# Kernel tuning notes

Hardware: AMD Instinct MI355X
Metric: run time of the kernel (lower is better)

## Reference

```python
import jax, jax.numpy as jnp
import numpy as np

N = 100000
E = 6400000
NT_DIM = 8
HID = 32


def setup_inputs() -> dict:
    key = jax.random.key(0)
    k1, k2, k3, k4, k5, k6, k7 = jax.random.split(key, 7)
    nt_emb = jax.random.normal(k1, (N, NT_DIM), dtype=jnp.float32)
    edge_index = jax.random.randint(k2, (2, E), 0, N, dtype=jnp.int64)
    lm_mask = jax.random.uniform(k3, (N,), dtype=jnp.float32)
    fan_in1 = 2 * NT_DIM + 2
    lim1 = 1.0 / np.sqrt(fan_in1)
    W1 = jax.random.uniform(k4, (fan_in1, HID), minval=-lim1, maxval=lim1, dtype=jnp.float32)
    b1 = jax.random.uniform(k5, (HID,), minval=-lim1, maxval=lim1, dtype=jnp.float32)
    lim2 = 1.0 / np.sqrt(HID)
    W2 = jax.random.uniform(k6, (HID, 1), minval=-lim2, maxval=lim2, dtype=jnp.float32)
    b2 = jax.random.uniform(k7, (1,), minval=-lim2, maxval=lim2, dtype=jnp.float32)
    return {"nt_emb": nt_emb, "edge_index": edge_index, "lm_mask": lm_mask,
            "W1": W1, "b1": b1, "W2": W2, "b2": b2}


def reference(nt_emb, edge_index, lm_mask, W1, b1, W2, b2):
    s, d = edge_index[0], edge_index[1]
    # [E, 2*nt_dim + 2] edge features: src emb, dst emb, src mask, dst mask
    feat = jnp.concatenate(
        [nt_emb[s], nt_emb[d], lm_mask[s][:, None], lm_mask[d][:, None]], axis=-1)
    h = jax.nn.relu(feat @ W1 + b1)          # [E, hid]
    out = jax.nn.sigmoid(h @ W2 + b2)        # [E, 1]
    return out[:, 0]                         # [E]
```

## Files before the change

### kernel.cpp

```cpp
#include <hip/hip_runtime.h>
#include <hip/hip_bf16.h>

typedef short short8 __attribute__((ext_vector_type(8)));
typedef float floatx4 __attribute__((ext_vector_type(4)));
typedef float floatx16 __attribute__((ext_vector_type(16)));

#define HID 32
#define NTD 8
#define FAN_IN 18

__device__ __forceinline__ short f2bf(float f) {
    union { float f; unsigned u; } v; v.f = f;
    unsigned r = v.u + 0x7fffu + ((v.u >> 16) & 1u);
    return (short)(r >> 16);
}

__device__ __forceinline__ float fast_sigmoid(float x) {
    float e = __builtin_amdgcn_exp2f(x * -1.44269504f);
    return __builtin_amdgcn_rcpf(1.0f + e);
}

__global__ void build_table(const float* __restrict__ emb,
                            const float* __restrict__ mask,
                            short* __restrict__ T, int N) {
    int n = blockIdx.x * blockDim.x + threadIdx.x;
    if (n >= N) return;
    const float4* p = (const float4*)(emb + (size_t)n * NTD);
    float4 lo = p[0], hi = p[1];
    short8 a, b;
    a[0] = f2bf(lo.x); a[1] = f2bf(lo.y); a[2] = f2bf(lo.z); a[3] = f2bf(lo.w);
    a[4] = f2bf(hi.x); a[5] = f2bf(hi.y); a[6] = f2bf(hi.z); a[7] = f2bf(hi.w);
    b[0] = f2bf(mask[n]); b[1] = (short)0x3F80;
    b[2] = b[3] = b[4] = b[5] = b[6] = b[7] = 0;
    short8* row = (short8*)(T + (size_t)n * 16);
    row[0] = a; row[1] = b;
}


__device__ __forceinline__ void make_frags(int4 lo, int4 hi, int h,
                                           short8& sf, short8& df) {
    int4 s4, d4;
    #pragma unroll
    for (int j = 0; j < 4; ++j) {
        int a = (&lo.x)[j];
        int b = (&hi.x)[j];
        int as = __shfl_xor(a, 32, 64);
        int bs = __shfl_xor(b, 32, 64);
        (&s4.x)[j] = h ? bs : a;
        (&d4.x)[j] = h ? b : as;
    }
    sf = __builtin_bit_cast(short8, s4);
    df = __builtin_bit_cast(short8, d4);
}

template <int ESZ>
__device__ __forceinline__ unsigned ld_idx(const char* __restrict__ idxBase,
                                           unsigned grp, unsigned nGroups,
                                           unsigned E, unsigned off, unsigned cc) {
    unsigned g = grp < nGroups ? grp : nGroups - 1u;
    unsigned e = g * 64u + off + cc;
    if (e >= E) e = E - 1u;
    return *(const unsigned*)(idxBase + (size_t)e * ESZ);
}

template <int ESZ>
__device__ void run32(const char* __restrict__ ei,
                      const char* __restrict__ Tc,
                      float* __restrict__ out, unsigned E,
                      short8 as, short8 ad, const float* __restrict__ w2r, float bias2,
                      unsigned waveId, unsigned nWaves, int h, int c, int lane) {
    const unsigned nGroups = (E + 63u) >> 6;
    const char* idxBase = ei + (h ? (size_t)E * ESZ : 0);
    const unsigned cc = (unsigned)c;

    if (waveId >= nGroups) return;
    unsigned cur = waveId;

    unsigned iA = ld_idx<ESZ>(idxBase, cur, nGroups, E, 0u, cc);
    unsigned iB = ld_idx<ESZ>(idxBase, cur, nGroups, E, 32u, cc);
    int4 loA = *(const int4*)(Tc + iA * 32u);
    int4 hiA = *(const int4*)(Tc + iA * 32u + 16u);
    int4 loB = *(const int4*)(Tc + iB * 32u);
    int4 hiB = *(const int4*)(Tc + iB * 32u + 16u);
    unsigned nA = ld_idx<ESZ>(idxBase, cur + nWaves, nGroups, E, 0u, cc);
    unsigned nB = ld_idx<ESZ>(idxBase, cur + nWaves, nGroups, E, 32u, cc);

    while (true) {
        int4 nloA = *(const int4*)(Tc + nA * 32u);
        int4 nhiA = *(const int4*)(Tc + nA * 32u + 16u);
        int4 nloB = *(const int4*)(Tc + nB * 32u);
        int4 nhiB = *(const int4*)(Tc + nB * 32u + 16u);
        unsigned nnA = ld_idx<ESZ>(idxBase, cur + 2u * nWaves, nGroups, E, 0u, cc);
        unsigned nnB = ld_idx<ESZ>(idxBase, cur + 2u * nWaves, nGroups, E, 32u, cc);

        short8 sfA, dfA, sfB, dfB;
        make_frags(loA, hiA, h, sfA, dfA);
        make_frags(loB, hiB, h, sfB, dfB);

        floatx16 accA = {0.f,0.f,0.f,0.f,0.f,0.f,0.f,0.f,0.f,0.f,0.f,0.f,0.f,0.f,0.f,0.f};
        floatx16 accB = accA;
        accA = __builtin_amdgcn_mfma_f32_32x32x16_bf16(as, sfA, accA, 0, 0, 0);
        accB = __builtin_amdgcn_mfma_f32_32x32x16_bf16(as, sfB, accB, 0, 0, 0);
        accA = __builtin_amdgcn_mfma_f32_32x32x16_bf16(ad, dfA, accA, 0, 0, 0);
        accB = __builtin_amdgcn_mfma_f32_32x32x16_bf16(ad, dfB, accB, 0, 0, 0);

        float pA0 = 0.f, pA1 = 0.f, pB0 = 0.f, pB1 = 0.f;
        #pragma unroll
        for (int q = 0; q < 16; q += 2) {
            pA0 += fmaxf(accA[q],     0.f) * w2r[q];
            pA1 += fmaxf(accA[q + 1], 0.f) * w2r[q + 1];
            pB0 += fmaxf(accB[q],     0.f) * w2r[q];
            pB1 += fmaxf(accB[q + 1], 0.f) * w2r[q + 1];
        }
        float pA = pA0 + pA1;
        float pB = pB0 + pB1;
        pA += __shfl_xor(pA, 32, 64);
        pB += __shfl_xor(pB, 32, 64);
        float vA = fast_sigmoid(pA + bias2);
        float vB = fast_sigmoid(pB + bias2);

        float v = (h == 0) ? vA : vB;
        unsigned e = (cur << 6) + (unsigned)lane;
        if (e < E) out[e] = v;

        cur += nWaves;
        if (cur >= nGroups) break;
        loA = nloA; hiA = nhiA; loB = nloB; hiB = nhiB;
        nA = nnA; nB = nnB;
    }
}

__global__ __launch_bounds__(256, 4) void lg_table_kernel(
    const char* __restrict__ ei_bytes,
    const short* __restrict__ T,
    const float* __restrict__ W1,
    const float* __restrict__ b1,
    const float* __restrict__ W2,
    const float* __restrict__ b2,
    float* __restrict__ out,
    long long E)
{
    const int lane = threadIdx.x & 63;
    const int waveInBlock = threadIdx.x >> 6;
    const unsigned waveId = (unsigned)(blockIdx.x * (blockDim.x >> 6) + waveInBlock);
    const unsigned nWaves = (unsigned)(gridDim.x * (blockDim.x >> 6));

    const int* ei32 = (const int*)ei_bytes;
    int probe = ei32[2 * lane + 1];
    unsigned long long nz = __ballot(probe != 0);
    const int esz = (nz == 0ull) ? 8 : 4;

    const int c = lane & 31;
    const int h = lane >> 5;

    short8 as, ad;
    #pragma unroll
    for (int j = 0; j < 8; ++j) {
        float vs = 0.f, vd = 0.f;
        if (h == 0) {
            vs = W1[j * HID + c];
            vd = W1[(8 + j) * HID + c];
        } else {
            if (j == 0) { vs = W1[16 * HID + c]; vd = W1[17 * HID + c]; }
            else if (j == 1) { vs = b1[c]; }
        }
        as[j] = f2bf(vs);
        ad[j] = f2bf(vd);
    }

    float w2r[16];
    #pragma unroll
    for (int q = 0; q < 16; ++q)
        w2r[q] = W2[(q & 3) + 8 * (q >> 2) + 4 * h];

    const float bias2 = b2[0];

    if (esz == 8)
        run32<8>(ei_bytes, (const char*)T, out, (unsigned)E, as, ad, w2r, bias2,
                 waveId, nWaves, h, c, lane);
    else
        run32<4>(ei_bytes, (const char*)T, out, (unsigned)E, as, ad, w2r, bias2,
                 waveId, nWaves, h, c, lane);
}

__global__ __launch_bounds__(256, 4) void lg_kernel(
    const float* __restrict__ nt_emb,
    const char* __restrict__ ei_bytes,
    const float* __restrict__ lm_mask,
    const float* __restrict__ W1,
    const float* __restrict__ b1,
    const float* __restrict__ W2,
    const float* __restrict__ b2,
    float* __restrict__ out,
    long long E)
{
    const int lane = threadIdx.x & 63;
    const int waveInBlock = threadIdx.x >> 6;
    const long long waveId = (long long)blockIdx.x * (blockDim.x >> 6) + waveInBlock;
    const long long nWaves = (long long)gridDim.x * (blockDim.x >> 6);

    const int* ei32 = (const int*)ei_bytes;
    int probe = ei32[2 * lane + 1];
    unsigned long long nz = __ballot(probe != 0);
    const long long esz = (nz == 0ull) ? 8 : 4;

    const int r = lane & 15;
    const int g = lane >> 4;

    short8 a0, a1;
    #pragma unroll
    for (int j = 0; j < 8; ++j) {
        int k = g * 8 + j;
        float v0 = 0.f, v1 = 0.f;
        if (k < FAN_IN)       { v0 = W1[k * HID + r];      v1 = W1[k * HID + 16 + r]; }
        else if (k == FAN_IN) { v0 = b1[r];                v1 = b1[16 + r]; }
        a0[j] = f2bf(v0);
        a1[j] = f2bf(v1);
    }

    float w2v0[4], w2v1[4];
    #pragma unroll
    for (int q = 0; q < 4; ++q) {
        w2v0[q] = W2[g * 4 + q];
        w2v1[q] = W2[16 + g * 4 + q];
    }
    const float bias2 = b2[0];

    const long long nGroups = (E + 15) >> 4;
    for (long long grp = waveId; grp < nGroups; grp += nWaves) {
        long long e = (grp << 4) + r;
        const bool valid = (e < E);
        long long ec = valid ? e : (E - 1);

        int s = *(const int*)(ei_bytes + ec * esz);
        int d = *(const int*)(ei_bytes + (E + ec) * esz);

        short8 fb;
        #pragma unroll
        for (int j = 0; j < 8; ++j) fb[j] = 0;
        if (g < 2) {
            const float4* p = (const float4*)(nt_emb + (long long)(g == 0 ? s : d) * NTD);
            float4 lo = p[0];
            float4 hi = p[1];
            fb[0] = f2bf(lo.x); fb[1] = f2bf(lo.y); fb[2] = f2bf(lo.z); fb[3] = f2bf(lo.w);
            fb[4] = f2bf(hi.x); fb[5] = f2bf(hi.y); fb[6] = f2bf(hi.z); fb[7] = f2bf(hi.w);
        } else if (g == 2) {
            fb[0] = f2bf(lm_mask[s]);
            fb[1] = f2bf(lm_mask[d]);
            fb[2] = (short)0x3F80;
        }

        floatx4 acc0 = {0.f, 0.f, 0.f, 0.f};
        floatx4 acc1 = {0.f, 0.f, 0.f, 0.f};
        acc0 = __builtin_amdgcn_mfma_f32_16x16x32_bf16(a0, fb, acc0, 0, 0, 0);
        acc1 = __builtin_amdgcn_mfma_f32_16x16x32_bf16(a1, fb, acc1, 0, 0, 0);

        float partial = 0.f;
        #pragma unroll
        for (int q = 0; q < 4; ++q) {
            partial += fmaxf(acc0[q], 0.f) * w2v0[q];
            partial += fmaxf(acc1[q], 0.f) * w2v1[q];
        }
        partial += __shfl_xor(partial, 16, 64);
        partial += __shfl_xor(partial, 32, 64);

        float val = fast_sigmoid(partial + bias2);
        if (g == 0 && valid) out[e] = val;
    }
}

extern "C" void kernel_launch(void* const* d_in, const int* in_sizes, int n_in,
                              void* d_out, int out_size, void* d_ws, size_t ws_size,
                              hipStream_t stream) {
    const float* nt_emb = (const float*)d_in[0];
    const char*  ei     = (const char*)d_in[1];
    const float* lm     = (const float*)d_in[2];
    const float* W1     = (const float*)d_in[3];
    const float* b1     = (const float*)d_in[4];
    const float* W2     = (const float*)d_in[5];
    const float* b2     = (const float*)d_in[6];
    float* out = (float*)d_out;

    long long E = (long long)in_sizes[1] / 2;
    int N = in_sizes[2];

    size_t tableBytes = (size_t)N * 32;
    if (ws_size >= tableBytes) {
        short* T = (short*)d_ws;
        build_table<<<dim3((N + 255) / 256), dim3(256), 0, stream>>>(nt_emb, lm, T, N);
        lg_table_kernel<<<dim3(2048), dim3(256), 0, stream>>>(ei, T, W1, b1, W2, b2, out, E);
    } else {
        lg_kernel<<<dim3(2048), dim3(256), 0, stream>>>(nt_emb, ei, lm, W1, b1, W2, b2, out, E);
    }
}
```

Before: 83.28 us.

## Pack node table into 16-byte rows with mask bits stolen from bf16 LSBs

The per-node gather table shrinks from 32 to 16 bytes by rounding embeddings to 15-bit bf16 and storing an 8-bit quantized mask in their low bits. Each edge lane now gathers one 16-byte row instead of two, and the MFMA fragments are rebuilt with only a mask shuffle. The W1 fragment layout is rearranged to match. This halves random-gather traffic at the cost of reduced embedding precision and an 8-bit mask quantization, plus some extra ALU for decoding.

```diff
diff --git a/kernel.cpp b/kernel.cpp
--- a/kernel.cpp
+++ b/kernel.cpp
@@ -15,6 +15,13 @@
     return (short)(r >> 16);
 }
 
+__device__ __forceinline__ unsigned short pack_emb(float f, unsigned bit) {
+    union { float f; unsigned u; } v; v.f = f;
+    unsigned r = v.u + 0xFFFFu + ((v.u >> 17) & 1u);
+    unsigned short s = (unsigned short)((r >> 16) & 0xFFFEu);
+    return (unsigned short)(s | bit);
+}
+
 __device__ __forceinline__ float fast_sigmoid(float x) {
     float e = __builtin_amdgcn_exp2f(x * -1.44269504f);
     return __builtin_amdgcn_rcpf(1.0f + e);
@@ -22,45 +29,76 @@
 
 __global__ void build_table(const float* __restrict__ emb,
                             const float* __restrict__ mask,
-                            short* __restrict__ T, int N) {
+                            unsigned short* __restrict__ T, int N) {
     int n = blockIdx.x * blockDim.x + threadIdx.x;
     if (n >= N) return;
     const float4* p = (const float4*)(emb + (size_t)n * NTD);
     float4 lo = p[0], hi = p[1];
-    short8 a, b;
-    a[0] = f2bf(lo.x); a[1] = f2bf(lo.y); a[2] = f2bf(lo.z); a[3] = f2bf(lo.w);
-    a[4] = f2bf(hi.x); a[5] = f2bf(hi.y); a[6] = f2bf(hi.z); a[7] = f2bf(hi.w);
-    b[0] = f2bf(mask[n]); b[1] = (short)0x3F80;
-    b[2] = b[3] = b[4] = b[5] = b[6] = b[7] = 0;
-    short8* row = (short8*)(T + (size_t)n * 16);
-    row[0] = a; row[1] = b;
-}
-
-
-__device__ __forceinline__ void make_frags(int4 lo, int4 hi, int h,
-                                           short8& sf, short8& df) {
-    int4 s4, d4;
-    #pragma unroll
-    for (int j = 0; j < 4; ++j) {
-        int a = (&lo.x)[j];
-        int b = (&hi.x)[j];
-        int as = __shfl_xor(a, 32, 64);
-        int bs = __shfl_xor(b, 32, 64);
-        (&s4.x)[j] = h ? bs : a;
-        (&d4.x)[j] = h ? b : as;
-    }
-    sf = __builtin_bit_cast(short8, s4);
-    df = __builtin_bit_cast(short8, d4);
-}
+    float ev[8] = {lo.x, lo.y, lo.z, lo.w, hi.x, hi.y, hi.z, hi.w};
+    float mf = mask[n] * 255.0f + 0.5f;
+    unsigned m8 = (unsigned)mf; if (m8 > 255u) m8 = 255u;
+    unsigned short row[8];
+    #pragma unroll
+    for (int j = 0; j < 8; ++j)
+        row[j] = pack_emb(ev[j], (m8 >> j) & 1u);
+    int4 out;
+    out.x = (int)((unsigned)row[0] | ((unsigned)row[1] << 16));
+    out.y = (int)((unsigned)row[2] | ((unsigned)row[3] << 16));
+    out.z = (int)((unsigned)row[4] | ((unsigned)row[5] << 16));
+    out.w = (int)((unsigned)row[6] | ((unsigned)row[7] << 16));
+    *(int4*)(T + (size_t)n * 8) = out;
+}
+
+__device__ __forceinline__ unsigned decode_m8(int4 r) {
+    unsigned m;
+    m  = ((unsigned)r.x & 1u);
+    m |= (((unsigned)r.x >> 16) & 1u) << 1;
+    m |= ((unsigned)r.y & 1u) << 2;
+    m |= (((unsigned)r.y >> 16) & 1u) << 3;
+    m |= ((unsigned)r.z & 1u) << 4;
+    m |= (((unsigned)r.z >> 16) & 1u) << 5;
+    m |= ((unsigned)r.w & 1u) << 6;
+    m |= (((unsigned)r.w >> 16) & 1u) << 7;
+    return m;
+}
+
 
 template <int ESZ>
-__device__ __forceinline__ unsigned ld_idx(const char* __restrict__ idxBase,
-                                           unsigned grp, unsigned nGroups,
-                                           unsigned E, unsigned off, unsigned cc) {
+__device__ __forceinline__ uint2 ld_idx2(const char* __restrict__ idxBase,
+                                         unsigned grp, unsigned nGroups,
+                                         unsigned E, unsigned cc) {
     unsigned g = grp < nGroups ? grp : nGroups - 1u;
-    unsigned e = g * 64u + off + cc;
-    if (e >= E) e = E - 1u;
-    return *(const unsigned*)(idxBase + (size_t)e * ESZ);
+    unsigned eA = g * 64u + cc;
+    unsigned eB = eA + 32u;
+    if (eA >= E) eA = E - 1u;
+    if (eB >= E) eB = E - 1u;
+    uint2 r;
+    r.x = *(const unsigned*)(idxBase + (size_t)eA * ESZ);
+    r.y = *(const unsigned*)(idxBase + (size_t)eB * ESZ);
+    return r;
+}
+
+__device__ __forceinline__ int4 grow(const char* __restrict__ Tc, unsigned idx) {
+    return *(const int4*)(Tc + (size_t)idx * 16u);
+}
+
+__device__ __forceinline__ void tile_frags(int4 row, int h, short8& fb1, short8& fb2) {
+    unsigned m8 = decode_m8(row);
+    unsigned m8p = (unsigned)__shfl_xor((int)m8, 32, 64);
+    float mfv = (float)m8p * (1.0f / 255.0f);
+    unsigned mbf = (unsigned)(unsigned short)f2bf(mfv);
+    int4 b1i, b2i;
+    if (h) {
+        b1i.x = (int)(mbf | 0x3F800000u);
+        b1i.y = 0; b1i.z = 0; b1i.w = 0;
+        b2i = row;
+    } else {
+        b1i = row;
+        b2i.x = (int)mbf;
+        b2i.y = 0; b2i.z = 0; b2i.w = 0;
+    }
+    fb1 = __builtin_bit_cast(short8, b1i);
+    fb2 = __builtin_bit_cast(short8, b2i);
 }
 
 template <int ESZ>
@@ -76,33 +114,26 @@
     if (waveId >= nGroups) return;
     unsigned cur = waveId;
 
-    unsigned iA = ld_idx<ESZ>(idxBase, cur, nGroups, E, 0u, cc);
-    unsigned iB = ld_idx<ESZ>(idxBase, cur, nGroups, E, 32u, cc);
-    int4 loA = *(const int4*)(Tc + iA * 32u);
-    int4 hiA = *(const int4*)(Tc + iA * 32u + 16u);
-    int4 loB = *(const int4*)(Tc + iB * 32u);
-    int4 hiB = *(const int4*)(Tc + iB * 32u + 16u);
-    unsigned nA = ld_idx<ESZ>(idxBase, cur + nWaves, nGroups, E, 0u, cc);
-    unsigned nB = ld_idx<ESZ>(idxBase, cur + nWaves, nGroups, E, 32u, cc);
+    uint2 i0 = ld_idx2<ESZ>(idxBase, cur, nGroups, E, cc);
+    int4 rA = grow(Tc, i0.x);
+    int4 rB = grow(Tc, i0.y);
+    uint2 i1 = ld_idx2<ESZ>(idxBase, cur + nWaves, nGroups, E, cc);
 
     while (true) {
-        int4 nloA = *(const int4*)(Tc + nA * 32u);
-        int4 nhiA = *(const int4*)(Tc + nA * 32u + 16u);
-        int4 nloB = *(const int4*)(Tc + nB * 32u);
-        int4 nhiB = *(const int4*)(Tc + nB * 32u + 16u);
-        unsigned nnA = ld_idx<ESZ>(idxBase, cur + 2u * nWaves, nGroups, E, 0u, cc);
-        unsigned nnB = ld_idx<ESZ>(idxBase, cur + 2u * nWaves, nGroups, E, 32u, cc);
-
-        short8 sfA, dfA, sfB, dfB;
-        make_frags(loA, hiA, h, sfA, dfA);
-        make_frags(loB, hiB, h, sfB, dfB);
+        int4 nA = grow(Tc, i1.x);
+        int4 nB = grow(Tc, i1.y);
+        uint2 i2 = ld_idx2<ESZ>(idxBase, cur + 2u * nWaves, nGroups, E, cc);
+
+        short8 fb1A, fb2A, fb1B, fb2B;
+        tile_frags(rA, h, fb1A, fb2A);
+        tile_frags(rB, h, fb1B, fb2B);
 
         floatx16 accA = {0.f,0.f,0.f,0.f,0.f,0.f,0.f,0.f,0.f,0.f,0.f,0.f,0.f,0.f,0.f,0.f};
         floatx16 accB = accA;
-        accA = __builtin_amdgcn_mfma_f32_32x32x16_bf16(as, sfA, accA, 0, 0, 0);
-        accB = __builtin_amdgcn_mfma_f32_32x32x16_bf16(as, sfB, accB, 0, 0, 0);
-        accA = __builtin_amdgcn_mfma_f32_32x32x16_bf16(ad, dfA, accA, 0, 0, 0);
-        accB = __builtin_amdgcn_mfma_f32_32x32x16_bf16(ad, dfB, accB, 0, 0, 0);
+        accA = __builtin_amdgcn_mfma_f32_32x32x16_bf16(as, fb1A, accA, 0, 0, 0);
+        accB = __builtin_amdgcn_mfma_f32_32x32x16_bf16(as, fb1B, accB, 0, 0, 0);
+        accA = __builtin_amdgcn_mfma_f32_32x32x16_bf16(ad, fb2A, accA, 0, 0, 0);
+        accB = __builtin_amdgcn_mfma_f32_32x32x16_bf16(ad, fb2B, accB, 0, 0, 0);
 
         float pA0 = 0.f, pA1 = 0.f, pB0 = 0.f, pB1 = 0.f;
         #pragma unroll
@@ -125,14 +156,14 @@
 
         cur += nWaves;
         if (cur >= nGroups) break;
-        loA = nloA; hiA = nhiA; loB = nloB; hiB = nhiB;
-        nA = nnA; nB = nnB;
+        rA = nA; rB = nB;
+        i1 = i2;
     }
 }
 
 __global__ __launch_bounds__(256, 4) void lg_table_kernel(
     const char* __restrict__ ei_bytes,
-    const short* __restrict__ T,
+    const unsigned short* __restrict__ T,
     const float* __restrict__ W1,
     const float* __restrict__ b1,
     const float* __restrict__ W2,
@@ -159,10 +190,11 @@
         float vs = 0.f, vd = 0.f;
         if (h == 0) {
             vs = W1[j * HID + c];
+            if (j == 0) vd = W1[17 * HID + c];
+        } else {
+            if (j == 0) vs = W1[16 * HID + c];
+            else if (j == 1) vs = b1[c];
             vd = W1[(8 + j) * HID + c];
-        } else {
-            if (j == 0) { vs = W1[16 * HID + c]; vd = W1[17 * HID + c]; }
-            else if (j == 1) { vs = b1[c]; }
         }
         as[j] = f2bf(vs);
         ad[j] = f2bf(vd);
@@ -284,9 +316,9 @@
     long long E = (long long)in_sizes[1] / 2;
     int N = in_sizes[2];
 
-    size_t tableBytes = (size_t)N * 32;
+    size_t tableBytes = (size_t)N * 16;
     if (ws_size >= tableBytes) {
-        short* T = (short*)d_ws;
+        unsigned short* T = (unsigned short*)d_ws;
         build_table<<<dim3((N + 255) / 256), dim3(256), 0, stream>>>(nt_emb, lm, T, N);
         lg_table_kernel<<<dim3(2048), dim3(256), 0, stream>>>(ei, T, W1, b1, W2, b2, out, E);
     } else {
```

After: 74.51 us, median of 4. 10.5% less time.
